# Optimization experiments

Hardware: AMD Instinct MI355X
Metric: run time of the kernel (lower is better)

Reference implementation:

```python
import jax, jax.numpy as jnp
import numpy as np
import math

D_MODEL = 512
D_STATE = 64  # N; state uses N//2 complex modes
BATCH = 8
SEQ = 4096
DT_MIN, DT_MAX = 1e-3, 1e-1


def setup_inputs() -> dict:
    key = jax.random.key(0)
    ks = jax.random.split(key, 8)
    H, N2 = D_MODEL, D_STATE // 2
    x = jax.random.normal(ks[0], (BATCH, SEQ, D_MODEL), dtype=jnp.float32)
    log_dt = jax.random.uniform(ks[1], (H,), dtype=jnp.float32) * (math.log(DT_MAX) - math.log(DT_MIN)) + math.log(DT_MIN)
    # A = -0.5 + i*pi*n  ->  A_real_log = log(0.5)
    A_real_log = jnp.full((H, N2), math.log(0.5), dtype=jnp.float32)
    A_imag = jnp.tile(jnp.arange(N2, dtype=jnp.float32) * math.pi, (H, 1))
    B_re = jax.random.normal(ks[2], (H, N2), dtype=jnp.float32)
    B_im = jax.random.normal(ks[3], (H, N2), dtype=jnp.float32)
    C_re = jax.random.normal(ks[4], (H, N2), dtype=jnp.float32)
    C_im = jax.random.normal(ks[5], (H, N2), dtype=jnp.float32)
    D = jax.random.normal(ks[6], (H,), dtype=jnp.float32)
    return {"x": x, "log_dt": log_dt, "A_real_log": A_real_log, "A_imag": A_imag,
            "B_re": B_re, "B_im": B_im, "C_re": C_re, "C_im": C_im, "D": D}


def _s4d_scan(x, log_dt, A_real_log, A_imag, B_re, B_im, C_re, C_im, D):
    # ZOH discretization (setup_step)
    dt = jnp.exp(log_dt)                                 # (H,)
    A = -jnp.exp(A_real_log) + 1j * A_imag               # (H, N2) complex
    dtA = A * dt[:, None]
    dA = jnp.exp(dtA)                                    # (H, N2)
    Bc = B_re + 1j * B_im
    Cc = C_re + 1j * C_im
    dB = Bc * (jnp.expm1(dtA) / A)                       # (H, N2)

    Bsz = x.shape[0]
    state0 = jnp.zeros((Bsz, x.shape[2], dA.shape[1]), dtype=jnp.complex64)

    def step(state, x_t):  # x_t: (B, H)
        state = dA * state + dB * x_t[..., None]         # (B, H, N2)
        y = 2.0 * jnp.real(jnp.einsum('hn,bhn->bh', Cc, state)) + D * x_t
        return state, jax.nn.gelu(y, approximate=False)

    final_state, ys = jax.lax.scan(step, state0, jnp.swapaxes(x, 0, 1))  # ys: (L, B, H)
    return jnp.swapaxes(ys, 0, 1), final_state


def reference(x, log_dt, A_real_log, A_imag, B_re, B_im, C_re, C_im, D):
    return _s4d_scan(x, log_dt, A_real_log, A_imag, B_re, B_im, C_re, C_im, D)
```

## Files before the change

### kernel.cpp

```cpp
#include <hip/hip_runtime.h>
#include <math.h>


#define H_  512
#define L_  4096
#define B_  8
#define N2_ 32
#define NC  64
#define THREADS 256
#define COLS 256
#define RSTR 72

typedef _Float16 f16;
typedef _Float16 f16x8 __attribute__((ext_vector_type(8)));
typedef _Float16 f16x4 __attribute__((ext_vector_type(4)));
typedef float    f32x4 __attribute__((ext_vector_type(4)));

__device__ __forceinline__ float bfly1(float v) {
    return __int_as_float(__builtin_amdgcn_update_dpp(
        0, __float_as_int(v), 0xB1, 0xf, 0xf, true));
}

__global__ __launch_bounds__(256) void k_trin(
    const float* __restrict__ x, f16* __restrict__ xT)
{
    __shared__ float tl[64][65];
    const int bid = (int)blockIdx.x;
    const int tt = bid & 63, hh = (bid >> 6) & 7, b = bid >> 9;
    const int t0 = tt * 64, h0 = hh * 64;
    const int tid = threadIdx.x;

    const float* src = x + ((size_t)b * L_ + t0) * H_ + h0;
#pragma unroll
    for (int i = 0; i < 4; ++i) {
        const int e = i * 256 + tid;
        const int t = e >> 4, hq = e & 15;
        const f32x4 v = *(const f32x4*)&src[(size_t)t * H_ + hq * 4];
#pragma unroll
        for (int j = 0; j < 4; ++j) tl[hq * 4 + j][t] = v[j];
    }
    __syncthreads();
#pragma unroll
    for (int i = 0; i < 2; ++i) {
        const int e = i * 256 + tid;
        const int hI = e >> 3, tq = e & 7;
        f16x8 pk;
#pragma unroll
        for (int j = 0; j < 8; ++j) pk[j] = (f16)tl[hI][tq * 8 + j];
        *(f16x8*)&xT[((size_t)(h0 + hI) * B_ + b) * L_ + t0 + tq * 8] = pk;
    }
}

__global__ __launch_bounds__(256) void k_trout(
    const f16* __restrict__ yT, float* __restrict__ y)
{
    __shared__ float tl[64][65];
    const int bid = (int)blockIdx.x;
    const int tt = bid & 63, hh = (bid >> 6) & 7, b = bid >> 9;
    const int t0 = tt * 64, h0 = hh * 64;
    const int tid = threadIdx.x;

#pragma unroll
    for (int i = 0; i < 2; ++i) {
        const int e = i * 256 + tid;
        const int hI = e >> 3, tq = e & 7;
        const f16x8 v = *(const f16x8*)
            &yT[((size_t)(h0 + hI) * B_ + b) * L_ + t0 + tq * 8];
#pragma unroll
        for (int j = 0; j < 8; ++j) tl[tq * 8 + j][hI] = (float)v[j];
    }
    __syncthreads();
    float* dst = y + ((size_t)b * L_ + t0) * H_ + h0;
#pragma unroll
    for (int i = 0; i < 4; ++i) {
        const int e = i * 256 + tid;
        const int t = e >> 4, hq = e & 15;
        f32x4 v;
#pragma unroll
        for (int j = 0; j < 4; ++j) v[j] = tl[t][hq * 4 + j];
        *(f32x4*)&dst[(size_t)t * H_ + hq * 4] = v;
    }
}

__global__ __launch_bounds__(THREADS, 2) void s4d_conv_kernel(
    const f16*  __restrict__ xT,
    const float* __restrict__ log_dt,
    const float* __restrict__ A_real_log,
    const float* __restrict__ A_imag,
    const float* __restrict__ B_re,
    const float* __restrict__ B_im,
    const float* __restrict__ C_re,
    const float* __restrict__ C_im,
    const float* __restrict__ Dv,
    f16*  __restrict__ yT,
    float* __restrict__ st_re,
    float* __restrict__ st_im)
{
    __shared__ f16 Xl[COLS][RSTR];
    __shared__ f16 PU[COLS][RSTR];
    __shared__ float s_xr[32], s_xi[32], s_dBr[32], s_dBi[32],
                     s_wr[32], s_wi[32], s_wdr[32], s_wdi[32],
                     s_Lr[32], s_Li[32], s_k[64];

    const int bid = (int)blockIdx.x;
    const int li  = bid >> 3;
    const int h   = (bid & 7) * 64 + (li >> 1);
    const int bh  = li & 1;

    const int tid = threadIdx.x;
    const int l   = tid & 63;
    const int w   = tid >> 6;

    if (tid < 32) {
        const int n = tid, hn = h * N2_ + n;
        const float dt = expf(log_dt[h]);
        const float Ar = -expf(A_real_log[hn]);
        const float Ai = A_imag[hn];
        const float xr = dt * Ar, xi = dt * Ai;
        s_xr[n] = xr; s_xi[n] = xi;
        const float ex = expf(xr), cs = cosf(xi), sn = sinf(xi);
        const float sh  = sinf(0.5f * xi);
        const float emr = expm1f(xr) * cs - 2.0f * sh * sh;
        const float emi = ex * sn;
        const float ia  = 1.0f / (Ar * Ar + Ai * Ai);
        const float tr  = (emr * Ar + emi * Ai) * ia;
        const float ti  = (emi * Ar - emr * Ai) * ia;
        const float Brv = B_re[hn], Biv = B_im[hn];
        const float dBr = Brv * tr - Biv * ti, dBi = Brv * ti + Biv * tr;
        s_dBr[n] = dBr; s_dBi[n] = dBi;
        const float wr = 2.0f * C_re[hn], wi = 2.0f * C_im[hn];
        s_wr[n] = wr; s_wi[n] = wi;
        s_wdr[n] = wr * dBr - wi * dBi;
        s_wdi[n] = wr * dBi + wi * dBr;
    }
    const float Dh = Dv[h];
    __syncthreads();

    float* pr = (float*)&PU[0][0];
    float* pi = pr + 32 * 66;
    for (int e = tid; e < 2048; e += THREADS) {
        const int n = e >> 6, p = e & 63;
        const float ex = expf((float)p * s_xr[n]);
        float sn, cs; sincosf((float)p * s_xi[n], &sn, &cs);
        pr[n * 66 + p] = ex * cs; pi[n * 66 + p] = ex * sn;
    }
    if (tid < 32) {
        const int n = tid;
        const float ex = expf(64.f * s_xr[n]);
        float sn, cs; sincosf(64.f * s_xi[n], &sn, &cs);
        pr[n * 66 + 64] = ex * cs; pi[n * 66 + 64] = ex * sn;
    }
    __syncthreads();

    if (tid < 64) {
        float acc = 0.f;
        for (int n = 0; n < 32; ++n)
            acc += s_wdr[n] * pr[n * 66 + tid] - s_wdi[n] * pi[n * 66 + tid];
        s_k[tid] = acc;
    }
    if (tid < 32) { s_Lr[tid] = pr[tid * 66 + 64]; s_Li[tid] = pi[tid * 66 + 64]; }
    for (int e = tid; e < 4096; e += THREADS) {
        const int t = e >> 6, j = e & 63, n = j >> 1;
        const float re = pr[n * 66 + t + 1], im = pi[n * 66 + t + 1];
        const float mv = (j & 1) ? -(s_wr[n] * im + s_wi[n] * re)
                                 :  (s_wr[n] * re - s_wi[n] * im);
        Xl[64 + t][j] = (f16)mv;
    }
    for (int e = tid; e < 4096; e += THREADS) {
        const int r = e >> 6, s = e & 63, n = r >> 1;
        const float re = pr[n * 66 + 63 - s], im = pi[n * 66 + 63 - s];
        const float vv = (r & 1) ? (s_dBr[n] * im + s_dBi[n] * re)
                                 : (s_dBr[n] * re - s_dBi[n] * im);
        Xl[128 + r][s] = (f16)vv;
    }
    __syncthreads();
    for (int e = tid; e < 4096; e += THREADS) {
        const int t = e >> 6, s = e & 63;
        Xl[t][s] = (f16)((s <= t) ? s_k[t - s] : 0.f);
    }
    __syncthreads();

    const int row16 = l & 15, kg = l >> 4;
    f16x8 Tf[4][2], Mf[4][2], Vf[4][2];
#pragma unroll
    for (int mt = 0; mt < 4; ++mt)
#pragma unroll
        for (int ks = 0; ks < 2; ++ks) {
            const int off = ks * 32 + kg * 8;
            Tf[mt][ks] = *(const f16x8*)&Xl[      mt * 16 + row16][off];
            Mf[mt][ks] = *(const f16x8*)&Xl[ 64 + mt * 16 + row16][off];
            Vf[mt][ks] = *(const f16x8*)&Xl[128 + mt * 16 + row16][off];
        }
    __syncthreads();

    {
        const int col = tid, b = bh * 4 + (col >> 6), c = col & 63;
        const f16* xg = xT + ((size_t)h * B_ + b) * L_ + (size_t)c * 64;
#pragma unroll
        for (int s0 = 0; s0 < 64; s0 += 8)
            *(f16x8*)&Xl[col][s0] = *(const f16x8*)&xg[s0];
    }
    __syncthreads();

    const int colbase = w * 64;

    f16x8 xbA[4], xbB[4];
#pragma unroll
    for (int nt = 0; nt < 4; ++nt) {
        const int col = colbase + nt * 16 + row16;
        xbA[nt] = *(const f16x8*)&Xl[col][kg * 8];
        xbB[nt] = *(const f16x8*)&Xl[col][32 + kg * 8];
        f32x4 ac0 = {0.f,0.f,0.f,0.f}, ac1 = {0.f,0.f,0.f,0.f},
              ac2 = {0.f,0.f,0.f,0.f}, ac3 = {0.f,0.f,0.f,0.f};
        ac0 = __builtin_amdgcn_mfma_f32_16x16x32_f16(Vf[0][0], xbA[nt], ac0, 0,0,0);
        ac0 = __builtin_amdgcn_mfma_f32_16x16x32_f16(Vf[0][1], xbB[nt], ac0, 0,0,0);
        ac1 = __builtin_amdgcn_mfma_f32_16x16x32_f16(Vf[1][0], xbA[nt], ac1, 0,0,0);
        ac1 = __builtin_amdgcn_mfma_f32_16x16x32_f16(Vf[1][1], xbB[nt], ac1, 0,0,0);
        ac2 = __builtin_amdgcn_mfma_f32_16x16x32_f16(Vf[2][0], xbA[nt], ac2, 0,0,0);
        ac2 = __builtin_amdgcn_mfma_f32_16x16x32_f16(Vf[2][1], xbB[nt], ac2, 0,0,0);
        ac3 = __builtin_amdgcn_mfma_f32_16x16x32_f16(Vf[3][0], xbA[nt], ac3, 0,0,0);
        ac3 = __builtin_amdgcn_mfma_f32_16x16x32_f16(Vf[3][1], xbB[nt], ac3, 0,0,0);
        f32x4 a4[4] = {ac0, ac1, ac2, ac3};
#pragma unroll
        for (int mt = 0; mt < 4; ++mt) {
            f16x4 pv;
            pv[0] = (f16)a4[mt][0]; pv[1] = (f16)a4[mt][1];
            pv[2] = (f16)a4[mt][2]; pv[3] = (f16)a4[mt][3];
            *(f16x4*)&PU[col][mt * 16 + kg * 4] = pv;
        }
    }

    {
        const int j = l, n = j >> 1;
        const float lr  = s_Lr[n];
        const float lis = (j & 1) ? s_Li[n] : -s_Li[n];
        float u = 0.f;
        for (int c = 0; c < NC; ++c) {
            const int col = colbase + c;
            const float pv = (float)PU[col][j];
            PU[col][j] = (f16)u;
            const float usw = bfly1(u);
            u = fmaf(lr, u, fmaf(lis, usw, pv));
        }
        const int pairIdx = (bh * 4 + w) * H_ + h;
        if ((j & 1) == 0) st_re[(size_t)pairIdx * N2_ + n] = u;
        else              st_im[(size_t)pairIdx * N2_ + n] = u;
    }

    {
        const int b = bh * 4 + w;
        f16* yb = yT + ((size_t)h * B_ + b) * L_;
#pragma unroll
        for (int nt = 0; nt < 4; ++nt) {
            const int col = colbase + nt * 16 + row16;
            const int cc  = nt * 16 + row16;
            const f16x8 ub0 = *(const f16x8*)&PU[col][kg * 8];
            const f16x8 ub1 = *(const f16x8*)&PU[col][32 + kg * 8];
#pragma unroll
            for (int mt = 0; mt < 4; ++mt) {
                f32x4 ac = {0.f, 0.f, 0.f, 0.f};
                ac = __builtin_amdgcn_mfma_f32_16x16x32_f16(Tf[mt][0], xbA[nt], ac, 0,0,0);
                ac = __builtin_amdgcn_mfma_f32_16x16x32_f16(Tf[mt][1], xbB[nt], ac, 0,0,0);
                ac = __builtin_amdgcn_mfma_f32_16x16x32_f16(Mf[mt][0], ub0, ac, 0,0,0);
                ac = __builtin_amdgcn_mfma_f32_16x16x32_f16(Mf[mt][1], ub1, ac, 0,0,0);
                const int t0 = mt * 16 + kg * 4;
                const f16x4 xs = *(const f16x4*)&Xl[col][t0];
                f16x4 pk;
#pragma unroll
                for (int r = 0; r < 4; ++r) {
                    const float y  = fmaf(Dh, (float)xs[r], ac[r]);
                    const float y2 = y * y;
                    const float arg = y * fmaf(-0.10294502f, y2, -2.30218425f);
                    const float e   = __builtin_amdgcn_exp2f(arg);
                    pk[r] = (f16)(y * __builtin_amdgcn_rcpf(1.0f + e));
                }
                *(f16x4*)&yb[(size_t)cc * 64 + t0] = pk;
            }
        }
    }
}

extern "C" void kernel_launch(void* const* d_in, const int* in_sizes, int n_in,
                              void* d_out, int out_size, void* d_ws, size_t ws_size,
                              hipStream_t stream) {
    (void)in_sizes; (void)n_in; (void)out_size; (void)ws_size;
    const float* x    = (const float*)d_in[0];
    const float* ldt  = (const float*)d_in[1];
    const float* Arl  = (const float*)d_in[2];
    const float* Aim  = (const float*)d_in[3];
    const float* Bre  = (const float*)d_in[4];
    const float* Bim  = (const float*)d_in[5];
    const float* Cre  = (const float*)d_in[6];
    const float* Cim  = (const float*)d_in[7];
    const float* Dv   = (const float*)d_in[8];
    float* out = (float*)d_out;
    float* st_re = out + (size_t)B_ * L_ * H_;
    float* st_im = st_re + (size_t)B_ * H_ * N2_;

    f16* xT = (f16*)out;
    f16* yT = (f16*)d_ws;

    hipLaunchKernelGGL(k_trin, dim3(64 * 8 * B_), dim3(256), 0, stream, x, xT);
    hipLaunchKernelGGL(s4d_conv_kernel, dim3(1024), dim3(THREADS), 0, stream,
                       xT, ldt, Arl, Aim, Bre, Bim, Cre, Cim, Dv,
                       yT, st_re, st_im);
    hipLaunchKernelGGL(k_trout, dim3(64 * 8 * B_), dim3(256), 0, stream,
                       yT, out);
}
```

Baseline: 175.0 us.

## Precompute per-channel convolution matrices in a separate kernel, batch the recurrence loads

Moves the per-channel construction of the Toeplitz, state-output and input-state matrices plus the chunk decay into a new kernel that runs once per channel and writes them to scratch space in the output buffer. Before this, each of the two batch-half blocks per channel rebuilt them. The main kernel now just copies them into shared memory. The sequential chunk recurrence also loads eight partial values ahead before the dependent FMA chain, to hide LDS latency. This adds an extra launch and a global round trip for the matrices.

```diff
diff --git a/kernel.cpp b/kernel.cpp
--- a/kernel.cpp
+++ b/kernel.cpp
@@ -82,8 +82,7 @@
     }
 }
 
-__global__ __launch_bounds__(THREADS, 2) void s4d_conv_kernel(
-    const f16*  __restrict__ xT,
+__global__ __launch_bounds__(256) void k_build(
     const float* __restrict__ log_dt,
     const float* __restrict__ A_real_log,
     const float* __restrict__ A_imag,
@@ -91,25 +90,14 @@
     const float* __restrict__ B_im,
     const float* __restrict__ C_re,
     const float* __restrict__ C_im,
-    const float* __restrict__ Dv,
-    f16*  __restrict__ yT,
-    float* __restrict__ st_re,
-    float* __restrict__ st_im)
+    f16*  __restrict__ G,
+    float* __restrict__ Lg)
 {
-    __shared__ f16 Xl[COLS][RSTR];
-    __shared__ f16 PU[COLS][RSTR];
+    __shared__ float pr[32 * 66], pi[32 * 66];
     __shared__ float s_xr[32], s_xi[32], s_dBr[32], s_dBi[32],
-                     s_wr[32], s_wi[32], s_wdr[32], s_wdi[32],
-                     s_Lr[32], s_Li[32], s_k[64];
-
-    const int bid = (int)blockIdx.x;
-    const int li  = bid >> 3;
-    const int h   = (bid & 7) * 64 + (li >> 1);
-    const int bh  = li & 1;
-
+                     s_wr[32], s_wi[32], s_wdr[32], s_wdi[32], s_k[64];
+    const int h   = (int)blockIdx.x;
     const int tid = threadIdx.x;
-    const int l   = tid & 63;
-    const int w   = tid >> 6;
 
     if (tid < 32) {
         const int n = tid, hn = h * N2_ + n;
@@ -133,12 +121,9 @@
         s_wdr[n] = wr * dBr - wi * dBi;
         s_wdi[n] = wr * dBi + wi * dBr;
     }
-    const float Dh = Dv[h];
-    __syncthreads();
-
-    float* pr = (float*)&PU[0][0];
-    float* pi = pr + 32 * 66;
-    for (int e = tid; e < 2048; e += THREADS) {
+    __syncthreads();
+
+    for (int e = tid; e < 2048; e += 256) {
         const int n = e >> 6, p = e & 63;
         const float ex = expf((float)p * s_xr[n]);
         float sn, cs; sincosf((float)p * s_xi[n], &sn, &cs);
@@ -158,25 +143,67 @@
             acc += s_wdr[n] * pr[n * 66 + tid] - s_wdi[n] * pi[n * 66 + tid];
         s_k[tid] = acc;
     }
-    if (tid < 32) { s_Lr[tid] = pr[tid * 66 + 64]; s_Li[tid] = pi[tid * 66 + 64]; }
-    for (int e = tid; e < 4096; e += THREADS) {
+    if (tid < 32) {
+        Lg[h * 64 + tid]      = pr[tid * 66 + 64];
+        Lg[h * 64 + 32 + tid] = pi[tid * 66 + 64];
+    }
+    f16* Gh = G + (size_t)h * 192 * 64;
+    for (int e = tid; e < 4096; e += 256) {
         const int t = e >> 6, j = e & 63, n = j >> 1;
         const float re = pr[n * 66 + t + 1], im = pi[n * 66 + t + 1];
         const float mv = (j & 1) ? -(s_wr[n] * im + s_wi[n] * re)
                                  :  (s_wr[n] * re - s_wi[n] * im);
-        Xl[64 + t][j] = (f16)mv;
-    }
-    for (int e = tid; e < 4096; e += THREADS) {
+        Gh[(size_t)(64 + t) * 64 + j] = (f16)mv;
+    }
+    for (int e = tid; e < 4096; e += 256) {
         const int r = e >> 6, s = e & 63, n = r >> 1;
         const float re = pr[n * 66 + 63 - s], im = pi[n * 66 + 63 - s];
         const float vv = (r & 1) ? (s_dBr[n] * im + s_dBi[n] * re)
                                  : (s_dBr[n] * re - s_dBi[n] * im);
-        Xl[128 + r][s] = (f16)vv;
-    }
-    __syncthreads();
-    for (int e = tid; e < 4096; e += THREADS) {
+        Gh[(size_t)(128 + r) * 64 + s] = (f16)vv;
+    }
+    __syncthreads();
+    for (int e = tid; e < 4096; e += 256) {
         const int t = e >> 6, s = e & 63;
-        Xl[t][s] = (f16)((s <= t) ? s_k[t - s] : 0.f);
+        Gh[(size_t)t * 64 + s] = (f16)((s <= t) ? s_k[t - s] : 0.f);
+    }
+}
+
+__global__ __launch_bounds__(THREADS, 2) void s4d_conv_kernel(
+    const f16*  __restrict__ xT,
+    const f16*  __restrict__ G,
+    const float* __restrict__ Lg,
+    const float* __restrict__ Dv,
+    f16*  __restrict__ yT,
+    float* __restrict__ st_re,
+    float* __restrict__ st_im)
+{
+    __shared__ f16 Xl[COLS][RSTR];
+    __shared__ f16 PU[COLS][RSTR];
+    __shared__ float s_Lr[32], s_Li[32];
+
+    const int bid = (int)blockIdx.x;
+    const int li  = bid >> 3;
+    const int h   = (bid & 7) * 64 + (li >> 1);
+    const int bh  = li & 1;
+
+    const int tid = threadIdx.x;
+    const int l   = tid & 63;
+    const int w   = tid >> 6;
+
+    const float Dh = Dv[h];
+
+    {
+        const f16* Gh = G + (size_t)h * 192 * 64;
+        for (int e = tid; e < 1536; e += THREADS) {
+            const int row = e >> 3, seg = e & 7;
+            *(f16x8*)&Xl[row][seg * 8] =
+                *(const f16x8*)&Gh[(size_t)row * 64 + seg * 8];
+        }
+        if (tid < 32) {
+            s_Lr[tid] = Lg[h * 64 + tid];
+            s_Li[tid] = Lg[h * 64 + 32 + tid];
+        }
     }
     __syncthreads();
 
@@ -235,12 +262,17 @@
         const float lr  = s_Lr[n];
         const float lis = (j & 1) ? s_Li[n] : -s_Li[n];
         float u = 0.f;
-        for (int c = 0; c < NC; ++c) {
-            const int col = colbase + c;
-            const float pv = (float)PU[col][j];
-            PU[col][j] = (f16)u;
-            const float usw = bfly1(u);
-            u = fmaf(lr, u, fmaf(lis, usw, pv));
+        for (int c0 = 0; c0 < NC; c0 += 8) {
+            float pv[8];
+#pragma unroll
+            for (int k2 = 0; k2 < 8; ++k2)
+                pv[k2] = (float)PU[colbase + c0 + k2][j];
+#pragma unroll
+            for (int k2 = 0; k2 < 8; ++k2) {
+                PU[colbase + c0 + k2][j] = (f16)u;
+                const float usw = bfly1(u);
+                u = fmaf(lr, u, fmaf(lis, usw, pv[k2]));
+            }
         }
         const int pairIdx = (bh * 4 + w) * H_ + h;
         if ((j & 1) == 0) st_re[(size_t)pairIdx * N2_ + n] = u;
@@ -297,13 +329,16 @@
     float* st_re = out + (size_t)B_ * L_ * H_;
     float* st_im = st_re + (size_t)B_ * H_ * N2_;
 
-    f16* xT = (f16*)out;
-    f16* yT = (f16*)d_ws;
+    f16*   xT = (f16*)out;
+    f16*   G  = (f16*)((char*)out + 33554432);
+    float* Lg = (float*)((char*)out + 33554432 + (size_t)H_ * 192 * 64 * 2);
+    f16*   yT = (f16*)d_ws;
 
     hipLaunchKernelGGL(k_trin, dim3(64 * 8 * B_), dim3(256), 0, stream, x, xT);
+    hipLaunchKernelGGL(k_build, dim3(H_), dim3(256), 0, stream,
+                       ldt, Arl, Aim, Bre, Bim, Cre, Cim, G, Lg);
     hipLaunchKernelGGL(s4d_conv_kernel, dim3(1024), dim3(THREADS), 0, stream,
-                       xT, ldt, Arl, Aim, Bre, Bim, Cre, Cim, Dv,
-                       yT, st_re, st_im);
+                       xT, G, Lg, Dv, yT, st_re, st_im);
     hipLaunchKernelGGL(k_trout, dim3(64 * 8 * B_), dim3(256), 0, stream,
                        yT, out);
 }
```

New measurement: 174.6 us. Within noise of the previous version (-0.3%).
